# Kernel tuning notes

Hardware: AMD Instinct MI355X
Metric: run time of the kernel (lower is better)

Reference implementation:

```python
import jax, jax.numpy as jnp
import numpy as np

FEAT = 128
N_RBF = 20
CUTOFF = 5.0
N_EDGES = 200000
N_CG = 2000


def _scatter_mean(src, idx, num):
    s = jax.ops.segment_sum(src, idx, num_segments=num)
    cnt = jax.ops.segment_sum(jnp.ones((src.shape[0],), src.dtype), idx, num_segments=num)
    cnt = jnp.maximum(cnt, 1.0).reshape((num,) + (1,) * (src.ndim - 1))
    return s / cnt


def setup_inputs() -> dict:
    key = jax.random.key(0)
    ks = jax.random.split(key, 8)
    s_i = jax.random.normal(ks[0], (N_EDGES, FEAT), jnp.float32)
    v_i = jax.random.normal(ks[1], (N_EDGES, FEAT, 3), jnp.float32)
    r_iI = jax.random.normal(ks[2], (N_EDGES, 3), jnp.float32)
    mapping = jax.random.randint(ks[3], (N_EDGES,), 0, N_CG)
    sc = 1.0 / np.sqrt(FEAT)
    W1 = jax.random.normal(ks[4], (FEAT, FEAT), jnp.float32) * sc
    b1 = jnp.zeros((FEAT,), jnp.float32)
    W2 = jax.random.normal(ks[5], (FEAT, 3 * FEAT), jnp.float32) * sc
    b2 = jnp.zeros((3 * FEAT,), jnp.float32)
    Wr = jax.random.normal(ks[6], (N_RBF, 3 * FEAT), jnp.float32) / np.sqrt(N_RBF)
    br = jnp.zeros((3 * FEAT,), jnp.float32)
    return dict(s_i=s_i, v_i=v_i, r_iI=r_iI, W1=W1, b1=b1, W2=W2, b2=b2,
                Wr=Wr, br=br, mapping=mapping, num_cg=N_CG)


def reference(s_i, v_i, r_iI, W1, b1, W2, b2, Wr, br, mapping, num_cg):
    # preprocess_r: eps added per component before the sum (faithful to source)
    dist = jnp.sqrt(jnp.sum(r_iI ** 2 + 1e-8, axis=-1))          # [E]
    unit = r_iI / dist[:, None]                                   # [E, 3]

    # inv_dense: Dense(F->F, swish) -> Dense(F->3F)
    phi = jax.nn.silu(s_i @ W1 + b1) @ W2 + b2                    # [E, 3F]

    # DistanceEmbed: PaiNN radial basis sin(n*pi*d/cutoff)/d -> Dense -> cosine envelope
    n = jnp.arange(1, N_RBF + 1, dtype=dist.dtype)
    d = dist[:, None]
    rbf = jnp.sin(n * jnp.pi * d / CUTOFF) / d                    # [E, n_rbf]
    env = jnp.where(dist < CUTOFF, 0.5 * (jnp.cos(jnp.pi * dist / CUTOFF) + 1.0), 0.0)
    w_s = (rbf @ Wr + br) * env[:, None]                          # [E, 3F]

    inv = (phi * w_s).reshape(-1, 3, FEAT)                        # [E, 3, F]
    split_0 = inv[:, 0, :][..., None]                             # [E, F, 1]
    split_1 = inv[:, 1, :]                                        # [E, F]
    split_2 = inv[:, 2, :][..., None]                             # [E, F, 1]

    delta_v_iI = split_2 * unit[:, None, :] + split_0 * v_i       # [E, F, 3]
    delta_s_iI = split_1                                          # [E, F]

    delta_v_I = _scatter_mean(delta_v_iI, mapping, num_cg)        # [n_cg, F, 3]
    delta_s_I = _scatter_mean(delta_s_iI, mapping, num_cg)        # [n_cg, F]
    return (delta_s_I, delta_v_I)
```

## Files before the change

kernel.cpp:

```cpp
#include <hip/hip_runtime.h>
#include <math.h>

#define FEATN 128
#define NRBF  20
#define NCG   2000
#define CUTF  5.0f
#define PI_F  3.14159265358979323846f

#define LSTR 136

typedef __attribute__((ext_vector_type(8))) short bf16x8;
typedef __attribute__((ext_vector_type(4))) float f32x4;

__device__ inline unsigned short f2bf(float x) {
    unsigned int u = __float_as_uint(x);
    u += 0x7fffu + ((u >> 16) & 1u);
    return (unsigned short)(u >> 16);
}

#define W1P_ELEMS (4*8*64*8)
#define W2P_ELEMS (4*24*64*8)
#define WRP_ELEMS (24*64*8)

__global__ void pack_weights(const float* __restrict__ W1,
                             const float* __restrict__ W2,
                             const float* __restrict__ Wr,
                             short* __restrict__ W1p,
                             short* __restrict__ W2p,
                             short* __restrict__ Wrp) {
    int t = blockIdx.x * blockDim.x + threadIdx.x;
    if (t < W1P_ELEMS) {
        int j = t & 7, lane = (t >> 3) & 63, tile = t >> 9;
        int nt = tile & 7, kt = tile >> 3;
        int k = kt * 32 + (lane >> 4) * 8 + j;
        int n = nt * 16 + (lane & 15);
        W1p[t] = (short)f2bf(W1[k * 128 + n]);
        return;
    }
    t -= W1P_ELEMS;
    if (t < W2P_ELEMS) {
        int j = t & 7, lane = (t >> 3) & 63, tile = t >> 9;
        int nt = tile % 24, kt = tile / 24;
        int k = kt * 32 + (lane >> 4) * 8 + j;
        int n = nt * 16 + (lane & 15);
        W2p[t] = (short)f2bf(W2[k * 384 + n]);
        return;
    }
    t -= WRP_ELEMS ? W2P_ELEMS : W2P_ELEMS;
    if (t < WRP_ELEMS) {
        int j = t & 7, lane = (t >> 3) & 63, nt = t >> 9;
        int k = (lane >> 4) * 8 + j;
        int n = nt * 16 + (lane & 15);
        float v = (k < NRBF) ? Wr[k * 384 + n] : 0.0f;
        Wrp[t] = (short)f2bf(v);
    }
}

__global__ void hist_kernel(const int* __restrict__ mapping,
                            int* __restrict__ counts, int E) {
    int t = blockIdx.x * blockDim.x + threadIdx.x;
    if (t < E) atomicAdd(&counts[mapping[t]], 1);
}

__global__ void scan_kernel(const int* __restrict__ counts,
                            int* __restrict__ start,
                            int* __restrict__ cursor) {
    int lane = threadIdx.x;
    int base = lane * 32;
    int loc[32];
    int s = 0;
#pragma unroll
    for (int j = 0; j < 32; ++j) {
        int idx = base + j;
        int c = (idx < NCG) ? counts[idx] : 0;
        loc[j] = s;
        s += c;
    }
    int inc = s;
#pragma unroll
    for (int off = 1; off < 64; off <<= 1) {
        int n = __shfl_up(inc, off, 64);
        if (lane >= off) inc += n;
    }
    int excl = inc - s;
#pragma unroll
    for (int j = 0; j < 32; ++j) {
        int idx = base + j;
        if (idx < NCG) {
            start[idx]  = excl + loc[j];
            cursor[idx] = excl + loc[j];
        }
    }
}

__global__ void scatter_kernel(const int* __restrict__ mapping,
                               int* __restrict__ cursor,
                               int* __restrict__ order, int E) {
    int t = blockIdx.x * blockDim.x + threadIdx.x;
    if (t < E) {
        int seg = mapping[t];
        int pos = atomicAdd(&cursor[seg], 1);
        order[pos] = t;
    }
}

__global__ __launch_bounds__(256, 4) void
main_kernel(const float* __restrict__ s_i, const float* __restrict__ v_i,
            const float* __restrict__ r_iI, const float* __restrict__ b1,
            const float* __restrict__ b2, const float* __restrict__ br,
            const int* __restrict__ order, const int* __restrict__ start,
            const int* __restrict__ counts,
            const short* __restrict__ W1p, const short* __restrict__ W2p,
            const short* __restrict__ Wrp,
            float* __restrict__ out) {
    __shared__ __align__(16) short lds_sh[64 * LSTR];
    __shared__ float lds_acc[4 * 512];
    __shared__ int   lds_eid[64];
    __shared__ float lds_dist[64];
    __shared__ float lds_env[64];
    __shared__ float lds_unit[64][3];

    const int tid  = threadIdx.x;
    const int lane = tid & 63;
    const int w    = tid >> 6;
    const int lq   = lane >> 4;
    const int lc   = lane & 15;
    const int seg  = blockIdx.x;

    const int st  = start[seg];
    const int cnt = counts[seg];

    for (int i = tid; i < 4 * 512; i += 256) lds_acc[i] = 0.0f;

    float b1v[8];
#pragma unroll
    for (int nt = 0; nt < 8; ++nt) b1v[nt] = b1[nt * 16 + lc];

    const bf16x8* W1f = reinterpret_cast<const bf16x8*>(W1p);
    const bf16x8* W2f = reinterpret_cast<const bf16x8*>(W2p);
    const bf16x8* Wrf = reinterpret_cast<const bf16x8*>(Wrp);

    const int nT = (cnt + 63) >> 6;
    for (int t = 0; t < nT; ++t) {
        const int base  = st + t * 64;
        const int valid = min(64, cnt - t * 64);

        __syncthreads();
        if (tid < 64) lds_eid[tid] = order[base + min(tid, valid - 1)];
        __syncthreads();

        {
            int row = tid >> 2;
            int q   = tid & 3;
            int e   = lds_eid[row];
            const float4* src = reinterpret_cast<const float4*>(
                s_i + (size_t)e * FEATN + q * 32);
            short* dst = lds_sh + row * LSTR + q * 32;
#pragma unroll
            for (int c = 0; c < 8; ++c) {
                float4 v = src[c];
                unsigned int p0 = (unsigned int)f2bf(v.x) | ((unsigned int)f2bf(v.y) << 16);
                unsigned int p1 = (unsigned int)f2bf(v.z) | ((unsigned int)f2bf(v.w) << 16);
                *reinterpret_cast<uint2*>(dst + c * 4) = make_uint2(p0, p1);
            }
        }
        if (tid < 64) {
            int e = lds_eid[tid];
            float x = r_iI[e * 3 + 0], y = r_iI[e * 3 + 1], z = r_iI[e * 3 + 2];
            float d = sqrtf(x * x + y * y + z * z + 3e-8f);
            lds_dist[tid] = d;
            float inv_d = 1.0f / d;
            lds_unit[tid][0] = x * inv_d;
            lds_unit[tid][1] = y * inv_d;
            lds_unit[tid][2] = z * inv_d;
            float env = (d < CUTF) ? 0.5f * (__cosf(PI_F * d / CUTF) + 1.0f) : 0.0f;
            lds_env[tid] = (tid < valid) ? env : 0.0f;
        }
        __syncthreads();

        bf16x8 a1[4];
#pragma unroll
        for (int kt = 0; kt < 4; ++kt)
            a1[kt] = *reinterpret_cast<const bf16x8*>(
                lds_sh + (w * 16 + lc) * LSTR + kt * 32 + lq * 8);

#pragma unroll
        for (int nt = 0; nt < 8; ++nt) {
            f32x4 acc = {0.f, 0.f, 0.f, 0.f};
#pragma unroll
            for (int kt = 0; kt < 4; ++kt)
                acc = __builtin_amdgcn_mfma_f32_16x16x32_bf16(
                    a1[kt], W1f[(kt * 8 + nt) * 64 + lane], acc, 0, 0, 0);
#pragma unroll
            for (int i = 0; i < 4; ++i) {
                float x = acc[i] + b1v[nt];
                float h = x / (1.0f + __expf(-x));
                lds_sh[(w * 16 + lq * 4 + i) * LSTR + nt * 16 + lc] = (short)f2bf(h);
            }
        }

        bf16x8 a2[4];
#pragma unroll
        for (int kt = 0; kt < 4; ++kt)
            a2[kt] = *reinterpret_cast<const bf16x8*>(
                lds_sh + (w * 16 + lc) * LSTR + kt * 32 + lq * 8);

        bf16x8 rb;
        {
            float d = lds_dist[w * 16 + lc];
            float inv_d = 1.0f / d;
            float x0 = PI_F * d / CUTF;
#pragma unroll
            for (int j = 0; j < 8; ++j) {
                int k = lq * 8 + j;
                float v = 0.0f;
                if (k < NRBF) v = __sinf((float)(k + 1) * x0) * inv_d;
                rb[j] = (short)f2bf(v);
            }
        }

        int   ei[4]; float envi[4], ux[4], uy[4], uz[4];
#pragma unroll
        for (int i = 0; i < 4; ++i) {
            int e = w * 16 + lq * 4 + i;
            ei[i]   = lds_eid[e];
            envi[i] = lds_env[e];
            ux[i] = lds_unit[e][0]; uy[i] = lds_unit[e][1]; uz[i] = lds_unit[e][2];
        }

        float* aw = lds_acc + w * 512;

#pragma unroll 1
        for (int ft = 0; ft < 8; ++ft) {
            f32x4 acc0 = {0.f,0.f,0.f,0.f}, acc1 = {0.f,0.f,0.f,0.f}, acc2 = {0.f,0.f,0.f,0.f};
#pragma unroll
            for (int kt = 0; kt < 4; ++kt) {
                bf16x8 a = a2[kt];
                acc0 = __builtin_amdgcn_mfma_f32_16x16x32_bf16(a, W2f[(kt * 24 + ft     ) * 64 + lane], acc0, 0, 0, 0);
                acc1 = __builtin_amdgcn_mfma_f32_16x16x32_bf16(a, W2f[(kt * 24 + ft +  8) * 64 + lane], acc1, 0, 0, 0);
                acc2 = __builtin_amdgcn_mfma_f32_16x16x32_bf16(a, W2f[(kt * 24 + ft + 16) * 64 + lane], acc2, 0, 0, 0);
            }
            f32x4 z4 = {0.f,0.f,0.f,0.f};
            f32x4 wa0 = __builtin_amdgcn_mfma_f32_16x16x32_bf16(rb, Wrf[(ft     ) * 64 + lane], z4, 0, 0, 0);
            f32x4 wa1 = __builtin_amdgcn_mfma_f32_16x16x32_bf16(rb, Wrf[(ft +  8) * 64 + lane], z4, 0, 0, 0);
            f32x4 wa2 = __builtin_amdgcn_mfma_f32_16x16x32_bf16(rb, Wrf[(ft + 16) * 64 + lane], z4, 0, 0, 0);

            int f = ft * 16 + lc;
            float b2v0 = b2[f], b2v1 = b2[128 + f], b2v2 = b2[256 + f];
            float brv0 = br[f], brv1 = br[128 + f], brv2 = br[256 + f];

            float sds = 0.f, svx = 0.f, svy = 0.f, svz = 0.f;
#pragma unroll
            for (int i = 0; i < 4; ++i) {
                float phi0 = acc0[i] + b2v0;
                float phi1 = acc1[i] + b2v1;
                float phi2 = acc2[i] + b2v2;
                float w0 = (wa0[i] + brv0) * envi[i];
                float w1 = (wa1[i] + brv1) * envi[i];
                float w2 = (wa2[i] + brv2) * envi[i];
                float inv0 = phi0 * w0;
                float inv1 = phi1 * w1;
                float inv2 = phi2 * w2;

                const float* vp = v_i + (size_t)ei[i] * 384 + f * 3;
                sds += inv1;
                svx += inv2 * ux[i] + inv0 * vp[0];
                svy += inv2 * uy[i] + inv0 * vp[1];
                svz += inv2 * uz[i] + inv0 * vp[2];
            }
            sds += __shfl_xor(sds, 16); sds += __shfl_xor(sds, 32);
            svx += __shfl_xor(svx, 16); svx += __shfl_xor(svx, 32);
            svy += __shfl_xor(svy, 16); svy += __shfl_xor(svy, 32);
            svz += __shfl_xor(svz, 16); svz += __shfl_xor(svz, 32);
            if (lq == 0) {
                aw[f]               += sds;
                aw[128 + f * 3 + 0] += svx;
                aw[128 + f * 3 + 1] += svy;
                aw[128 + f * 3 + 2] += svz;
            }
        }
    }
    __syncthreads();

    const float invc = (cnt > 0) ? (1.0f / (float)cnt) : 0.0f;
    const int NS = NCG * 128;
    for (int o = tid; o < 512; o += 256) {
        float v = lds_acc[o] + lds_acc[512 + o] + lds_acc[1024 + o] + lds_acc[1536 + o];
        v *= invc;
        if (o < 128) out[(size_t)seg * 128 + o] = v;
        else         out[NS + (size_t)seg * 384 + (o - 128)] = v;
    }
}

extern "C" void kernel_launch(void* const* d_in, const int* in_sizes, int n_in,
                              void* d_out, int out_size, void* d_ws, size_t ws_size,
                              hipStream_t stream) {
    const float* s_i  = (const float*)d_in[0];
    const float* v_i  = (const float*)d_in[1];
    const float* r_iI = (const float*)d_in[2];
    const float* W1   = (const float*)d_in[3];
    const float* b1   = (const float*)d_in[4];
    const float* W2   = (const float*)d_in[5];
    const float* b2   = (const float*)d_in[6];
    const float* Wr   = (const float*)d_in[7];
    const float* br   = (const float*)d_in[8];
    const int* mapping = (const int*)d_in[9];

    const int E = in_sizes[0] / FEATN;

    char* ws = (char*)d_ws;
    int*   counts = (int*)(ws + 0);
    int*   start  = (int*)(ws + 8192);
    int*   cursor = (int*)(ws + 16384);
    int*   order  = (int*)(ws + 24576);
    short* W1p    = (short*)(ws + 829440);
    short* W2p    = (short*)(ws + 862208);
    short* Wrp    = (short*)(ws + 960512);

    hipMemsetAsync(counts, 0, NCG * sizeof(int), stream);
    pack_weights<<<(W1P_ELEMS + W2P_ELEMS + WRP_ELEMS) / 256, 256, 0, stream>>>(
        W1, W2, Wr, W1p, W2p, Wrp);
    hist_kernel<<<(E + 255) / 256, 256, 0, stream>>>(mapping, counts, E);
    scan_kernel<<<1, 64, 0, stream>>>(counts, start, cursor);
    scatter_kernel<<<(E + 255) / 256, 256, 0, stream>>>(mapping, cursor, order, E);
    main_kernel<<<NCG, 256, 0, stream>>>(s_i, v_i, r_iI, b1, b2, br,
                                         order, start, counts,
                                         W1p, W2p, Wrp, (float*)d_out);
}
```

Before: 806.3 us.

## Prefetch next edge tile and double-buffer v_i loads with wave-private LDS

Loads of the next 64-edge tile (s_i rows, r_iI, gather indices) are issued into registers before the current tile's MFMA work and written to double-buffered LDS afterwards. Each wave now owns its own LDS rows, so the per-tile block barriers are dropped. v_i gathers for the next feature tile are issued ahead of the current one's math through a two-set register scheme. Biases are staged in LDS and MFMA sections get raised wave priority. The goal is to hide gather latency, at the cost of extra register pressure that may reduce occupancy.

```diff
diff --git a/kernel.cpp b/kernel.cpp
--- a/kernel.cpp
+++ b/kernel.cpp
@@ -46,7 +46,7 @@
         W2p[t] = (short)f2bf(W2[k * 384 + n]);
         return;
     }
-    t -= WRP_ELEMS ? W2P_ELEMS : W2P_ELEMS;
+    t -= W2P_ELEMS;
     if (t < WRP_ELEMS) {
         int j = t & 7, lane = (t >> 3) & 63, nt = t >> 9;
         int k = (lane >> 4) * 8 + j;
@@ -115,10 +115,11 @@
             float* __restrict__ out) {
     __shared__ __align__(16) short lds_sh[64 * LSTR];
     __shared__ float lds_acc[4 * 512];
-    __shared__ int   lds_eid[64];
-    __shared__ float lds_dist[64];
-    __shared__ float lds_env[64];
-    __shared__ float lds_unit[64][3];
+    __shared__ float lds_bias[768];
+    __shared__ int   lds_eid[2][64];
+    __shared__ float lds_dist[2][64];
+    __shared__ float lds_env[2][64];
+    __shared__ float lds_unit[2][64][3];
 
     const int tid  = threadIdx.x;
     const int lane = tid & 63;
@@ -130,7 +131,13 @@
     const int st  = start[seg];
     const int cnt = counts[seg];
 
+    const int  R   = w * 16 + (lane >> 2);
+    const int  sq  = lane & 3;
+    const bool geo = (lane < 16);
+    const int  G   = w * 16 + (lane & 15);
+
     for (int i = tid; i < 4 * 512; i += 256) lds_acc[i] = 0.0f;
+    for (int i = tid; i < 768; i += 256) lds_bias[i] = (i < 384) ? b2[i] : br[i - 384];
 
     float b1v[8];
 #pragma unroll
@@ -140,49 +147,77 @@
     const bf16x8* W2f = reinterpret_cast<const bf16x8*>(W2p);
     const bf16x8* Wrf = reinterpret_cast<const bf16x8*>(Wrp);
 
+    __syncthreads();
+
     const int nT = (cnt + 63) >> 6;
-    for (int t = 0; t < nT; ++t) {
-        const int base  = st + t * 64;
-        const int valid = min(64, cnt - t * 64);
-
-        __syncthreads();
-        if (tid < 64) lds_eid[tid] = order[base + min(tid, valid - 1)];
-        __syncthreads();
-
+
+    float4 sp[8];
+    int eg = 0; float gx = 0.f, gy = 0.f, gz = 0.f;
+
+    if (nT > 0) {
+        const int valid0 = min(64, cnt);
         {
-            int row = tid >> 2;
-            int q   = tid & 3;
-            int e   = lds_eid[row];
+            const int e0 = order[st + min(R, valid0 - 1)];
             const float4* src = reinterpret_cast<const float4*>(
-                s_i + (size_t)e * FEATN + q * 32);
-            short* dst = lds_sh + row * LSTR + q * 32;
+                s_i + (size_t)e0 * FEATN + sq * 32);
+#pragma unroll
+            for (int c = 0; c < 8; ++c) sp[c] = src[c];
+        }
+        if (geo) {
+            eg = order[st + min(G, valid0 - 1)];
+            gx = r_iI[(size_t)eg * 3 + 0];
+            gy = r_iI[(size_t)eg * 3 + 1];
+            gz = r_iI[(size_t)eg * 3 + 2];
+        }
+        {
+            short* dst = lds_sh + R * LSTR + sq * 32;
 #pragma unroll
             for (int c = 0; c < 8; ++c) {
-                float4 v = src[c];
+                float4 v = sp[c];
                 unsigned int p0 = (unsigned int)f2bf(v.x) | ((unsigned int)f2bf(v.y) << 16);
                 unsigned int p1 = (unsigned int)f2bf(v.z) | ((unsigned int)f2bf(v.w) << 16);
                 *reinterpret_cast<uint2*>(dst + c * 4) = make_uint2(p0, p1);
             }
         }
-        if (tid < 64) {
-            int e = lds_eid[tid];
-            float x = r_iI[e * 3 + 0], y = r_iI[e * 3 + 1], z = r_iI[e * 3 + 2];
-            float d = sqrtf(x * x + y * y + z * z + 3e-8f);
-            lds_dist[tid] = d;
+        if (geo) {
+            float d = sqrtf(gx * gx + gy * gy + gz * gz + 3e-8f);
             float inv_d = 1.0f / d;
-            lds_unit[tid][0] = x * inv_d;
-            lds_unit[tid][1] = y * inv_d;
-            lds_unit[tid][2] = z * inv_d;
+            lds_dist[0][G] = d;
+            lds_unit[0][G][0] = gx * inv_d;
+            lds_unit[0][G][1] = gy * inv_d;
+            lds_unit[0][G][2] = gz * inv_d;
             float env = (d < CUTF) ? 0.5f * (__cosf(PI_F * d / CUTF) + 1.0f) : 0.0f;
-            lds_env[tid] = (tid < valid) ? env : 0.0f;
-        }
-        __syncthreads();
+            lds_env[0][G] = (G < valid0) ? env : 0.0f;
+            lds_eid[0][G] = eg;
+        }
+    }
+
+    for (int t = 0; t < nT; ++t) {
+        const int p = t & 1;
 
         bf16x8 a1[4];
 #pragma unroll
         for (int kt = 0; kt < 4; ++kt)
             a1[kt] = *reinterpret_cast<const bf16x8*>(
                 lds_sh + (w * 16 + lc) * LSTR + kt * 32 + lq * 8);
+
+        const bool pf = (t + 1 < nT);
+        int validn = 0;
+        if (pf) {
+            validn = min(64, cnt - (t + 1) * 64);
+            const int basen = st + (t + 1) * 64;
+            const int e1 = order[basen + min(R, validn - 1)];
+            const float4* src = reinterpret_cast<const float4*>(
+                s_i + (size_t)e1 * FEATN + sq * 32);
+#pragma unroll
+            for (int c = 0; c < 8; ++c) sp[c] = src[c];
+            if (geo) {
+                eg = order[basen + min(G, validn - 1)];
+                gx = r_iI[(size_t)eg * 3 + 0];
+                gy = r_iI[(size_t)eg * 3 + 1];
+                gz = r_iI[(size_t)eg * 3 + 2];
+            }
+        }
 
 #pragma unroll
         for (int nt = 0; nt < 8; ++nt) {
@@ -207,7 +242,7 @@
 
         bf16x8 rb;
         {
-            float d = lds_dist[w * 16 + lc];
+            float d = lds_dist[p][w * 16 + lc];
             float inv_d = 1.0f / d;
             float x0 = PI_F * d / CUTF;
 #pragma unroll
@@ -219,66 +254,123 @@
             }
         }
 
-        int   ei[4]; float envi[4], ux[4], uy[4], uz[4];
+        float envi[4], ux[4], uy[4], uz[4];
+        unsigned voff[4];
 #pragma unroll
         for (int i = 0; i < 4; ++i) {
-            int e = w * 16 + lq * 4 + i;
-            ei[i]   = lds_eid[e];
-            envi[i] = lds_env[e];
-            ux[i] = lds_unit[e][0]; uy[i] = lds_unit[e][1]; uz[i] = lds_unit[e][2];
+            const int e = w * 16 + lq * 4 + i;
+            envi[i] = lds_env[p][e];
+            ux[i] = lds_unit[p][e][0];
+            uy[i] = lds_unit[p][e][1];
+            uz[i] = lds_unit[p][e][2];
+            voff[i] = (unsigned)lds_eid[p][e] * 1536u;
+        }
+
+        if (pf) {
+            short* dst = lds_sh + R * LSTR + sq * 32;
+#pragma unroll
+            for (int c = 0; c < 8; ++c) {
+                float4 v = sp[c];
+                unsigned int p0 = (unsigned int)f2bf(v.x) | ((unsigned int)f2bf(v.y) << 16);
+                unsigned int p1 = (unsigned int)f2bf(v.z) | ((unsigned int)f2bf(v.w) << 16);
+                *reinterpret_cast<uint2*>(dst + c * 4) = make_uint2(p0, p1);
+            }
+            if (geo) {
+                float d = sqrtf(gx * gx + gy * gy + gz * gz + 3e-8f);
+                float inv_d = 1.0f / d;
+                const int pn = p ^ 1;
+                lds_dist[pn][G] = d;
+                lds_unit[pn][G][0] = gx * inv_d;
+                lds_unit[pn][G][1] = gy * inv_d;
+                lds_unit[pn][G][2] = gz * inv_d;
+                float env = (d < CUTF) ? 0.5f * (__cosf(PI_F * d / CUTF) + 1.0f) : 0.0f;
+                lds_env[pn][G] = (G < validn) ? env : 0.0f;
+                lds_eid[pn][G] = eg;
+            }
         }
 
         float* aw = lds_acc + w * 512;
 
+#define LOADV(VX, VY, VZ, ftv)                                               \
+        if ((ftv) < 8) {                                                     \
+            const int f_ = (ftv) * 16 + lc;                                  \
+            _Pragma("unroll")                                                \
+            for (int i_ = 0; i_ < 4; ++i_) {                                 \
+                const float* vp_ = (const float*)((const char*)v_i +         \
+                                                  voff[i_] + f_ * 12);       \
+                VX[i_] = vp_[0]; VY[i_] = vp_[1]; VZ[i_] = vp_[2];           \
+            }                                                                \
+        }
+
+#define FTBODY(ftv, VX, VY, VZ) {                                            \
+            const int ft_ = (ftv);                                           \
+            f32x4 acc0 = {0.f,0.f,0.f,0.f}, acc1 = {0.f,0.f,0.f,0.f},        \
+                  acc2 = {0.f,0.f,0.f,0.f};                                  \
+            __builtin_amdgcn_s_setprio(1);                                   \
+            _Pragma("unroll")                                                \
+            for (int kt_ = 0; kt_ < 4; ++kt_) {                              \
+                bf16x8 a_ = a2[kt_];                                         \
+                acc0 = __builtin_amdgcn_mfma_f32_16x16x32_bf16(              \
+                    a_, W2f[(kt_ * 24 + ft_     ) * 64 + lane], acc0, 0,0,0);\
+                acc1 = __builtin_amdgcn_mfma_f32_16x16x32_bf16(              \
+                    a_, W2f[(kt_ * 24 + ft_ +  8) * 64 + lane], acc1, 0,0,0);\
+                acc2 = __builtin_amdgcn_mfma_f32_16x16x32_bf16(              \
+                    a_, W2f[(kt_ * 24 + ft_ + 16) * 64 + lane], acc2, 0,0,0);\
+            }                                                                \
+            f32x4 z4 = {0.f,0.f,0.f,0.f};                                    \
+            f32x4 wa0 = __builtin_amdgcn_mfma_f32_16x16x32_bf16(             \
+                rb, Wrf[(ft_     ) * 64 + lane], z4, 0, 0, 0);               \
+            f32x4 wa1 = __builtin_amdgcn_mfma_f32_16x16x32_bf16(             \
+                rb, Wrf[(ft_ +  8) * 64 + lane], z4, 0, 0, 0);               \
+            f32x4 wa2 = __builtin_amdgcn_mfma_f32_16x16x32_bf16(             \
+                rb, Wrf[(ft_ + 16) * 64 + lane], z4, 0, 0, 0);               \
+            __builtin_amdgcn_s_setprio(0);                                   \
+            const int f_ = ft_ * 16 + lc;                                    \
+            float b2v0 = lds_bias[f_], b2v1 = lds_bias[128 + f_],            \
+                  b2v2 = lds_bias[256 + f_];                                 \
+            float brv0 = lds_bias[384 + f_], brv1 = lds_bias[512 + f_],      \
+                  brv2 = lds_bias[640 + f_];                                 \
+            float sds = 0.f, svx = 0.f, svy = 0.f, svz = 0.f;                \
+            _Pragma("unroll")                                                \
+            for (int i_ = 0; i_ < 4; ++i_) {                                 \
+                float phi0 = acc0[i_] + b2v0;                                \
+                float phi1 = acc1[i_] + b2v1;                                \
+                float phi2 = acc2[i_] + b2v2;                                \
+                float w0 = (wa0[i_] + brv0) * envi[i_];                      \
+                float w1 = (wa1[i_] + brv1) * envi[i_];                      \
+                float w2 = (wa2[i_] + brv2) * envi[i_];                      \
+                float inv0 = phi0 * w0;                                      \
+                float inv1 = phi1 * w1;                                      \
+                float inv2 = phi2 * w2;                                      \
+                sds += inv1;                                                 \
+                svx += inv2 * ux[i_] + inv0 * VX[i_];                        \
+                svy += inv2 * uy[i_] + inv0 * VY[i_];                        \
+                svz += inv2 * uz[i_] + inv0 * VZ[i_];                        \
+            }                                                                \
+            sds += __shfl_xor(sds, 16); sds += __shfl_xor(sds, 32);          \
+            svx += __shfl_xor(svx, 16); svx += __shfl_xor(svx, 32);          \
+            svy += __shfl_xor(svy, 16); svy += __shfl_xor(svy, 32);          \
+            svz += __shfl_xor(svz, 16); svz += __shfl_xor(svz, 32);          \
+            if (lq == 0) {                                                   \
+                aw[f_]               += sds;                                 \
+                aw[128 + f_ * 3 + 0] += svx;                                 \
+                aw[128 + f_ * 3 + 1] += svy;                                 \
+                aw[128 + f_ * 3 + 2] += svz;                                 \
+            }                                                                \
+        }
+
+        float vAx[4], vAy[4], vAz[4], vBx[4], vBy[4], vBz[4];
+        LOADV(vAx, vAy, vAz, 0)
 #pragma unroll 1
-        for (int ft = 0; ft < 8; ++ft) {
-            f32x4 acc0 = {0.f,0.f,0.f,0.f}, acc1 = {0.f,0.f,0.f,0.f}, acc2 = {0.f,0.f,0.f,0.f};
-#pragma unroll
-            for (int kt = 0; kt < 4; ++kt) {
-                bf16x8 a = a2[kt];
-                acc0 = __builtin_amdgcn_mfma_f32_16x16x32_bf16(a, W2f[(kt * 24 + ft     ) * 64 + lane], acc0, 0, 0, 0);
-                acc1 = __builtin_amdgcn_mfma_f32_16x16x32_bf16(a, W2f[(kt * 24 + ft +  8) * 64 + lane], acc1, 0, 0, 0);
-                acc2 = __builtin_amdgcn_mfma_f32_16x16x32_bf16(a, W2f[(kt * 24 + ft + 16) * 64 + lane], acc2, 0, 0, 0);
-            }
-            f32x4 z4 = {0.f,0.f,0.f,0.f};
-            f32x4 wa0 = __builtin_amdgcn_mfma_f32_16x16x32_bf16(rb, Wrf[(ft     ) * 64 + lane], z4, 0, 0, 0);
-            f32x4 wa1 = __builtin_amdgcn_mfma_f32_16x16x32_bf16(rb, Wrf[(ft +  8) * 64 + lane], z4, 0, 0, 0);
-            f32x4 wa2 = __builtin_amdgcn_mfma_f32_16x16x32_bf16(rb, Wrf[(ft + 16) * 64 + lane], z4, 0, 0, 0);
-
-            int f = ft * 16 + lc;
-            float b2v0 = b2[f], b2v1 = b2[128 + f], b2v2 = b2[256 + f];
-            float brv0 = br[f], brv1 = br[128 + f], brv2 = br[256 + f];
-
-            float sds = 0.f, svx = 0.f, svy = 0.f, svz = 0.f;
-#pragma unroll
-            for (int i = 0; i < 4; ++i) {
-                float phi0 = acc0[i] + b2v0;
-                float phi1 = acc1[i] + b2v1;
-                float phi2 = acc2[i] + b2v2;
-                float w0 = (wa0[i] + brv0) * envi[i];
-                float w1 = (wa1[i] + brv1) * envi[i];
-                float w2 = (wa2[i] + brv2) * envi[i];
-                float inv0 = phi0 * w0;
-                float inv1 = phi1 * w1;
-                float inv2 = phi2 * w2;
-
-                const float* vp = v_i + (size_t)ei[i] * 384 + f * 3;
-                sds += inv1;
-                svx += inv2 * ux[i] + inv0 * vp[0];
-                svy += inv2 * uy[i] + inv0 * vp[1];
-                svz += inv2 * uz[i] + inv0 * vp[2];
-            }
-            sds += __shfl_xor(sds, 16); sds += __shfl_xor(sds, 32);
-            svx += __shfl_xor(svx, 16); svx += __shfl_xor(svx, 32);
-            svy += __shfl_xor(svy, 16); svy += __shfl_xor(svy, 32);
-            svz += __shfl_xor(svz, 16); svz += __shfl_xor(svz, 32);
-            if (lq == 0) {
-                aw[f]               += sds;
-                aw[128 + f * 3 + 0] += svx;
-                aw[128 + f * 3 + 1] += svy;
-                aw[128 + f * 3 + 2] += svz;
-            }
-        }
+        for (int fp = 0; fp < 4; ++fp) {
+            const int ft0 = fp * 2;
+            LOADV(vBx, vBy, vBz, ft0 + 1)
+            FTBODY(ft0, vAx, vAy, vAz)
+            LOADV(vAx, vAy, vAz, ft0 + 2)
+            FTBODY(ft0 + 1, vBx, vBy, vBz)
+        }
+#undef LOADV
+#undef FTBODY
     }
     __syncthreads();
 
```

After: 1.060 ms. 1.32x slower.
